# Performance work log

Hardware: AMD Instinct MI355X
Metric: run time of the kernel (lower is better)

## Reference

```python
import jax, jax.numpy as jnp
import numpy as np

B, M, D, N, P = 8, 4096, 1024, 64, 2
TEMP = 0.1
EPS = 1e-12  # torch F.normalize default eps


def setup_inputs() -> dict:
    key = jax.random.key(0)
    k1, k2, k3 = jax.random.split(key, 3)
    x = jax.random.normal(k1, (B, M, D), jnp.float32)
    # xavier_normal_(phi, gain=1.5): std = 1.5*sqrt(2/(fan_in+fan_out)) with fan_in=D, fan_out=N*P
    phi = jax.random.normal(k2, (D, N, P), jnp.float32) * np.float32(1.5 * np.sqrt(2.0 / (D + N * P)))
    scale = jnp.ones((1,), jnp.float32)
    W = jax.random.normal(k3, (N, D, D), jnp.float32) * np.float32(1.0 / np.sqrt(D))
    b = jnp.zeros((N, D), jnp.float32)
    return {"x": x, "phi": phi, "scale": scale, "W": W, "b": b}


def reference(x, phi, scale, W, b):
    # normalize tokens along feature dim, phi along dim 0 (like F.normalize)
    xn = x / jnp.maximum(jnp.linalg.norm(x, axis=2, keepdims=True), EPS)
    phin = scale * (phi / jnp.maximum(jnp.linalg.norm(phi, axis=0, keepdims=True), EPS))
    # router logits [b, m, n, p]
    logits = jnp.einsum('bmd,dnp->bmnp', xn, phin) / TEMP
    d = jax.nn.softmax(logits, axis=1)                    # dispatch: softmax over tokens m
    c = jax.nn.softmax(logits.reshape(B, M, N * P), axis=-1).reshape(B, M, N, P)  # combine: softmax over (n,p)
    xs = jnp.einsum('bmd,bmnp->bnpd', x, d)               # slot inputs [b, n, p, d]
    # per-expert Linear(dim, dim): batched over expert axis n
    ys = jnp.einsum('bnpd,nde->bnpe', xs, W) + b[None, :, None, :]
    y = jnp.einsum('bnpd,bmnp->bmd', ys, c)
    return y + x  # add_residual=True
```

## Files before the change

kernel.cpp:

```cpp
#include <hip/hip_runtime.h>
#include <hip/hip_bf16.h>
#include <math.h>

#define B_ 8
#define M_ 4096
#define D_ 1024
#define NP_ 128
#define TEMP_ 0.1f
#define EPS_ 1e-12f

typedef __attribute__((ext_vector_type(8))) short bf16x8;
typedef __attribute__((ext_vector_type(4))) float f32x4;

__device__ __forceinline__ unsigned short f2bf(float f) {
    union { float f; unsigned int u; } v; v.f = f;
    unsigned int u = v.u;
    u += 0x7fff + ((u >> 16) & 1);
    return (unsigned short)(u >> 16);
}

__device__ __forceinline__ void stage_tile(const char* gbase, size_t row_stride,
                                           char* lds, int tid) {
    const int lane = tid & 63, w = tid >> 6;
#pragma unroll
    for (int t = 0; t < 2; ++t) {
        const int row = w * 32 + t * 16 + (lane >> 2);
        const char* g = gbase + (size_t)row * row_stride + (lane & 3) * 16;
        char* l = lds + (w * 32 + t * 16) * 64 + lane * 16;
        __builtin_amdgcn_global_load_lds((const __attribute__((address_space(1))) unsigned int*)g,
                                         (__attribute__((address_space(3))) unsigned int*)l,
                                         16, 0, 0);
    }
}

__device__ __forceinline__ void stage_rows64(const char* gbase, size_t row_stride,
                                             char* lds, int tid) {
    const int lane = tid & 63, w = tid >> 6;
    const int row = w * 16 + (lane >> 2);
    const char* g = gbase + (size_t)row * row_stride + (lane & 3) * 16;
    char* l = lds + (w * 16) * 64 + lane * 16;
    __builtin_amdgcn_global_load_lds((const __attribute__((address_space(1))) unsigned int*)g,
                                     (__attribute__((address_space(3))) unsigned int*)l,
                                     16, 0, 0);
}

template <int NI, int NJ>
__device__ __forceinline__ void mfma_tile(const char* At, const char* Bt,
                                          f32x4 (&acc)[NI][NJ], int wm, int wn,
                                          int fr, int q) {
    bf16x8 a[NI], bb[NJ];
#pragma unroll
    for (int i = 0; i < NI; ++i)
        a[i] = *(const bf16x8*)(At + (wm + i * 16 + fr) * 64 + q * 16);
#pragma unroll
    for (int j = 0; j < NJ; ++j)
        bb[j] = *(const bf16x8*)(Bt + (wn + j * 16 + fr) * 64 + q * 16);
#pragma unroll
    for (int i = 0; i < NI; ++i)
#pragma unroll
        for (int j = 0; j < NJ; ++j)
            acc[i][j] = __builtin_amdgcn_mfma_f32_16x16x32_bf16(a[i], bb[j], acc[i][j], 0, 0, 0);
}

__global__ __launch_bounds__(256) void k_prepT(const float* __restrict__ x,
                                               unsigned short* __restrict__ xbf,
                                               unsigned short* __restrict__ xbfT,
                                               float* __restrict__ rinv) {
    const int p = blockIdx.x;
    const int b = p >> 6, m0 = (p & 63) * 64;
    const int tid = threadIdx.x;
    const int mg = tid >> 4;
    const int d4 = tid & 15;
    __shared__ unsigned short lt[2][64][72];
    float ss[4] = {0.f, 0.f, 0.f, 0.f};
    for (int ch = 0; ch < 16; ++ch) {
        const int d0 = ch * 64;
        const int buf = ch & 1;
#pragma unroll
        for (int ii = 0; ii < 4; ++ii) {
            const int m = mg + ii * 16;
            float4 v = *(const float4*)(x + ((size_t)(b * M_ + m0 + m)) * D_ + d0 + d4 * 4);
            ss[ii] += v.x * v.x + v.y * v.y + v.z * v.z + v.w * v.w;
            ushort4 bv;
            bv.x = f2bf(v.x); bv.y = f2bf(v.y); bv.z = f2bf(v.z); bv.w = f2bf(v.w);
            *(ushort4*)(xbf + ((size_t)(b * M_ + m0 + m)) * D_ + d0 + d4 * 4) = bv;
            lt[buf][d4 * 4 + 0][m] = bv.x;
            lt[buf][d4 * 4 + 1][m] = bv.y;
            lt[buf][d4 * 4 + 2][m] = bv.z;
            lt[buf][d4 * 4 + 3][m] = bv.w;
        }
        __syncthreads();
        const int dl = tid >> 2, mq = (tid & 3) * 16;
        bf16x8 v0 = *(const bf16x8*)&lt[buf][dl][mq];
        bf16x8 v1 = *(const bf16x8*)&lt[buf][dl][mq + 8];
        unsigned short* to = xbfT + ((size_t)(b * D_ + d0 + dl)) * M_ + m0 + mq;
        *(bf16x8*)(to) = v0;
        *(bf16x8*)(to + 8) = v1;
    }
#pragma unroll
    for (int ii = 0; ii < 4; ++ii) {
        float s = ss[ii];
        s += __shfl_down(s, 8, 16);
        s += __shfl_down(s, 4, 16);
        s += __shfl_down(s, 2, 16);
        s += __shfl_down(s, 1, 16);
        if (d4 == 0)
            rinv[b * M_ + m0 + mg + ii * 16] = 1.0f / (fmaxf(sqrtf(s), EPS_) * TEMP_);
    }
}

__global__ void k_phin(const float* __restrict__ phi, const float* __restrict__ scale,
                       unsigned short* __restrict__ phinT) {
    const int np = blockIdx.x, tid = threadIdx.x;
    float ss = 0.f;
    for (int d = tid; d < D_; d += 256) {
        float v = phi[d * NP_ + np];
        ss += v * v;
    }
    __shared__ float red[256];
    red[tid] = ss;
    __syncthreads();
    for (int s = 128; s > 0; s >>= 1) {
        if (tid < s) red[tid] += red[tid + s];
        __syncthreads();
    }
    float inv = scale[0] / fmaxf(sqrtf(red[0]), EPS_);
    for (int d = tid; d < D_; d += 256) phinT[np * D_ + d] = f2bf(phi[d * NP_ + np] * inv);
}

__global__ __launch_bounds__(256) void k_logits(const unsigned short* __restrict__ phinT,
                                                const unsigned short* __restrict__ xbf,
                                                const float* __restrict__ rinv,
                                                float* __restrict__ logitsT) {
    const int m0 = blockIdx.x * 64;
    const int np0 = blockIdx.y * 64;
    const int b = blockIdx.z;
    const int tid = threadIdx.x, lane = tid & 63, w = tid >> 6;
    __shared__ char At[2][4096], Bt[2][4096];
    f32x4 acc[2][2] = {};
    const char* abase = (const char*)(xbf + ((size_t)b * M_ + m0) * D_);
    const char* bbase = (const char*)(phinT + (size_t)np0 * D_);
    const int wmm = (w & 1) * 32, wnn = (w >> 1) * 32;
    const int fr = lane & 15, q = lane >> 4;
    stage_rows64(abase, 2048, At[0], tid);
    stage_rows64(bbase, 2048, Bt[0], tid);
    __syncthreads();
    int cur = 0;
    for (int k0 = 64; k0 < 2048; k0 += 64) {
        stage_rows64(abase + k0, 2048, At[cur ^ 1], tid);
        stage_rows64(bbase + k0, 2048, Bt[cur ^ 1], tid);
        mfma_tile<2, 2>(At[cur], Bt[cur], acc, wmm, wnn, fr, q);
        __syncthreads();
        cur ^= 1;
    }
    mfma_tile<2, 2>(At[cur], Bt[cur], acc, wmm, wnn, fr, q);
#pragma unroll
    for (int i = 0; i < 2; ++i) {
        const int mm = wmm + i * 16 + q * 4;
        const float4 rv = *(const float4*)(rinv + (size_t)b * M_ + m0 + mm);
#pragma unroll
        for (int j = 0; j < 2; ++j) {
            const int np = np0 + wnn + j * 16 + fr;
            float4 o;
            o.x = acc[i][j][0] * rv.x;
            o.y = acc[i][j][1] * rv.y;
            o.z = acc[i][j][2] * rv.z;
            o.w = acc[i][j][3] * rv.w;
            *(float4*)(logitsT + ((size_t)b * NP_ + np) * M_ + m0 + mm) = o;
        }
    }
}

__global__ void k_colstats(const float* __restrict__ logitsT, float* __restrict__ cmax,
                           float* __restrict__ cinv) {
    const int row = blockIdx.x * 4 + (threadIdx.x >> 6);
    const int lane = threadIdx.x & 63;
    const float4* base = (const float4*)(logitsT + (size_t)row * M_);
    float mx = -1e30f, sm = 0.f;
#pragma unroll 4
    for (int it = 0; it < 16; ++it) {
        float4 v = base[lane + 64 * it];
        float lm = fmaxf(fmaxf(v.x, v.y), fmaxf(v.z, v.w));
        float nm = fmaxf(mx, lm);
        sm = sm * __expf(mx - nm) + __expf(v.x - nm) + __expf(v.y - nm) + __expf(v.z - nm) +
             __expf(v.w - nm);
        mx = nm;
    }
    for (int off = 32; off > 0; off >>= 1) {
        float om = __shfl_down(mx, off), os = __shfl_down(sm, off);
        float nm = fmaxf(mx, om);
        sm = sm * __expf(mx - nm) + os * __expf(om - nm);
        mx = nm;
    }
    if (lane == 0) {
        cmax[row] = mx;
        cinv[row] = 1.0f / sm;
    }
}

__global__ __launch_bounds__(256) void k_weights(const float* __restrict__ logitsT,
                                                 const float* __restrict__ cmax,
                                                 const float* __restrict__ cinv,
                                                 unsigned short* __restrict__ dvalT,
                                                 unsigned short* __restrict__ cbf) {
    const int b = blockIdx.y, m0 = blockIdx.x * 32;
    const int tid = threadIdx.x;
    __shared__ float lt[128][36];
    __shared__ float red[32][8];
    __shared__ float rstat[32][2];
    const int np = tid >> 1;
    const int mh = (tid & 1) * 16;
    const float cm = cmax[b * NP_ + np], ci = cinv[b * NP_ + np];
    unsigned short ev[16];
#pragma unroll
    for (int ii = 0; ii < 4; ++ii) {
        const int mq = mh + ii * 4;
        float4 v = *(const float4*)(logitsT + ((size_t)b * NP_ + np) * M_ + m0 + mq);
        *(float4*)&lt[np][mq] = v;
        ev[ii * 4 + 0] = f2bf(__expf(v.x - cm) * ci);
        ev[ii * 4 + 1] = f2bf(__expf(v.y - cm) * ci);
        ev[ii * 4 + 2] = f2bf(__expf(v.z - cm) * ci);
        ev[ii * 4 + 3] = f2bf(__expf(v.w - cm) * ci);
    }
    {
        unsigned short* dp = dvalT + ((size_t)b * NP_ + np) * M_ + m0 + mh;
        *(bf16x8*)dp = *(const bf16x8*)&ev[0];
        *(bf16x8*)(dp + 8) = *(const bf16x8*)&ev[8];
    }
    __syncthreads();
    const int mm = tid >> 3, g = tid & 7;
    float mx = -1e30f;
#pragma unroll
    for (int i = 0; i < 16; ++i) mx = fmaxf(mx, lt[g * 16 + i][mm]);
    red[mm][g] = mx;
    __syncthreads();
    if (g == 0) {
        float M2 = red[mm][0];
#pragma unroll
        for (int k = 1; k < 8; ++k) M2 = fmaxf(M2, red[mm][k]);
        rstat[mm][0] = M2;
    }
    __syncthreads();
    const float rm = rstat[mm][0];
    float s = 0.f;
#pragma unroll
    for (int i = 0; i < 16; ++i) s += __expf(lt[g * 16 + i][mm] - rm);
    red[mm][g] = s;
    __syncthreads();
    if (g == 0) {
        float S = 0.f;
#pragma unroll
        for (int k = 0; k < 8; ++k) S += red[mm][k];
        rstat[mm][1] = 1.0f / S;
    }
    __syncthreads();
    const float ri = rstat[mm][1];
    bf16x8 o0, o1;
#pragma unroll
    for (int i = 0; i < 8; ++i) o0[i] = (short)f2bf(__expf(lt[g * 16 + i][mm] - rm) * ri);
#pragma unroll
    for (int i = 0; i < 8; ++i) o1[i] = (short)f2bf(__expf(lt[g * 16 + 8 + i][mm] - rm) * ri);
    unsigned short* co = cbf + ((size_t)b * M_ + m0 + mm) * NP_ + g * 16;
    *(bf16x8*)(co) = o0;
    *(bf16x8*)(co + 8) = o1;
}

__global__ __launch_bounds__(256) void k_xs(const unsigned short* __restrict__ dvalT,
                                            const unsigned short* __restrict__ xbfT,
                                            float* __restrict__ partial) {
    const int dt = blockIdx.x, kc = blockIdx.y, b = blockIdx.z;
    const int d0 = dt * 64;
    const int tid = threadIdx.x, lane = tid & 63, w = tid >> 6;
    __shared__ char At[2][4096], Bt[2][8192];
    f32x4 acc[2][4] = {};
    const char* abase = (const char*)(xbfT + ((size_t)b * D_ + d0) * M_) + (size_t)kc * 1024;
    const char* bbase = (const char*)(dvalT + (size_t)b * NP_ * M_) + (size_t)kc * 1024;
    const int wmm = (w & 1) * 32, wnn = (w >> 1) * 64;
    const int fr = lane & 15, q = lane >> 4;
    stage_rows64(abase, (size_t)M_ * 2, At[0], tid);
    stage_tile(bbase, (size_t)M_ * 2, Bt[0], tid);
    __syncthreads();
    int cur = 0;
    for (int k0 = 64; k0 < 1024; k0 += 64) {
        stage_rows64(abase + k0, (size_t)M_ * 2, At[cur ^ 1], tid);
        stage_tile(bbase + k0, (size_t)M_ * 2, Bt[cur ^ 1], tid);
        mfma_tile<2, 4>(At[cur], Bt[cur], acc, wmm, wnn, fr, q);
        __syncthreads();
        cur ^= 1;
    }
    mfma_tile<2, 4>(At[cur], Bt[cur], acc, wmm, wnn, fr, q);
#pragma unroll
    for (int i = 0; i < 2; ++i) {
        const int dd = d0 + wmm + i * 16 + q * 4;
#pragma unroll
        for (int j = 0; j < 4; ++j) {
            const int np = wnn + j * 16 + fr;
            float4 o;
            o.x = acc[i][j][0]; o.y = acc[i][j][1]; o.z = acc[i][j][2]; o.w = acc[i][j][3];
            *(float4*)(partial + (((size_t)kc * B_ + b) * NP_ + np) * D_ + dd) = o;
        }
    }
}

__global__ void k_xsred(const float* __restrict__ partial, float* __restrict__ xs) {
    const size_t i = ((size_t)blockIdx.x * 256 + threadIdx.x) * 4;
    const size_t CH = (size_t)B_ * NP_ * D_;
    float4 o = *(const float4*)(partial + i);
#pragma unroll
    for (int c = 1; c < 8; ++c) {
        float4 s = *(const float4*)(partial + (size_t)c * CH + i);
        o.x += s.x; o.y += s.y; o.z += s.z; o.w += s.w;
    }
    *(float4*)(xs + i) = o;
}

__global__ __launch_bounds__(256) void k_ys(const float* __restrict__ xs,
                                            const float* __restrict__ W,
                                            const float* __restrict__ bias,
                                            unsigned short* __restrict__ ysT) {
    const int et = blockIdx.x;
    const int n = blockIdx.y;
    const int e0 = et * 128;
    const int tid = threadIdx.x, tx = tid & 31, ty = tid >> 5;
    __shared__ float wt[32][128];
    __shared__ float xst[16][32];
    float acc[2][4];
#pragma unroll
    for (int j = 0; j < 2; ++j)
#pragma unroll
        for (int q = 0; q < 4; ++q) acc[j][q] = 0.f;
    const float* wbase = W + (size_t)n * D_ * D_;
    for (int k0 = 0; k0 < D_; k0 += 32) {
#pragma unroll
        for (int it = 0; it < 4; ++it) {
            int idx = tid + 256 * it;
            int row = idx >> 5, c4 = (idx & 31) * 4;
            *(float4*)(&wt[row][c4]) = *(const float4*)(wbase + (size_t)(k0 + row) * D_ + e0 + c4);
        }
        if (tid < 128) {
            int r = tid >> 3, c4 = (tid & 7) * 4;
            int bb = r >> 1, pp = r & 1;
            *(float4*)(&xst[r][c4]) =
                *(const float4*)(xs + ((size_t)bb * NP_ + n * 2 + pp) * D_ + k0 + c4);
        }
        __syncthreads();
#pragma unroll
        for (int k = 0; k < 32; ++k) {
            float4 w4 = *(const float4*)(&wt[k][tx * 4]);
            float r0 = xst[ty * 2][k], r1 = xst[ty * 2 + 1][k];
            acc[0][0] += r0 * w4.x; acc[0][1] += r0 * w4.y;
            acc[0][2] += r0 * w4.z; acc[0][3] += r0 * w4.w;
            acc[1][0] += r1 * w4.x; acc[1][1] += r1 * w4.y;
            acc[1][2] += r1 * w4.z; acc[1][3] += r1 * w4.w;
        }
        __syncthreads();
    }
    float4 bv = *(const float4*)(bias + n * D_ + e0 + tx * 4);
#pragma unroll
    for (int j = 0; j < 2; ++j) {
        const int r = ty * 2 + j;
        const int bb = r >> 1, pp = r & 1;
        float v0 = acc[j][0] + bv.x, v1 = acc[j][1] + bv.y;
        float v2 = acc[j][2] + bv.z, v3 = acc[j][3] + bv.w;
        ysT[((size_t)bb * D_ + e0 + tx * 4 + 0) * NP_ + n * 2 + pp] = f2bf(v0);
        ysT[((size_t)bb * D_ + e0 + tx * 4 + 1) * NP_ + n * 2 + pp] = f2bf(v1);
        ysT[((size_t)bb * D_ + e0 + tx * 4 + 2) * NP_ + n * 2 + pp] = f2bf(v2);
        ysT[((size_t)bb * D_ + e0 + tx * 4 + 3) * NP_ + n * 2 + pp] = f2bf(v3);
    }
}

__global__ __launch_bounds__(256) void k_final(const unsigned short* __restrict__ cbf,
                                               const unsigned short* __restrict__ ysT,
                                               const float* __restrict__ x,
                                               float* __restrict__ out) {
    const int et = blockIdx.x, mt = blockIdx.y, b = blockIdx.z;
    const int e0 = et * 128, m0 = mt * 128;
    const int tid = threadIdx.x, lane = tid & 63, w = tid >> 6;
    __shared__ char At[2][8192], Bt[2][8192];
    f32x4 acc[4][4] = {};
    const char* abase = (const char*)(ysT + ((size_t)b * D_ + e0) * NP_);
    const char* bbase = (const char*)(cbf + ((size_t)b * M_ + m0) * NP_);
    const int wmm = (w & 1) * 64, wnn = (w >> 1) * 64;
    const int fr = lane & 15, q = lane >> 4;
    stage_tile(abase, 256, At[0], tid);
    stage_tile(bbase, 256, Bt[0], tid);
    __syncthreads();
    int cur = 0;
    for (int k0 = 64; k0 < 256; k0 += 64) {
        stage_tile(abase + k0, 256, At[cur ^ 1], tid);
        stage_tile(bbase + k0, 256, Bt[cur ^ 1], tid);
        mfma_tile<4, 4>(At[cur], Bt[cur], acc, wmm, wnn, fr, q);
        __syncthreads();
        cur ^= 1;
    }
    mfma_tile<4, 4>(At[cur], Bt[cur], acc, wmm, wnn, fr, q);
#pragma unroll
    for (int i = 0; i < 4; ++i) {
        const int e = e0 + wmm + i * 16 + q * 4;
#pragma unroll
        for (int j = 0; j < 4; ++j) {
            const int m = m0 + wnn + j * 16 + fr;
            const size_t idx = ((size_t)b * M_ + m) * D_ + e;
            float4 xv = *(const float4*)(x + idx);
            float4 o;
            o.x = acc[i][j][0] + xv.x;
            o.y = acc[i][j][1] + xv.y;
            o.z = acc[i][j][2] + xv.z;
            o.w = acc[i][j][3] + xv.w;
            *(float4*)(out + idx) = o;
        }
    }
}

extern "C" void kernel_launch(void* const* d_in, const int* in_sizes, int n_in,
                              void* d_out, int out_size, void* d_ws, size_t ws_size,
                              hipStream_t stream) {
    const float* x = (const float*)d_in[0];
    const float* phi = (const float*)d_in[1];
    const float* scale = (const float*)d_in[2];
    const float* W = (const float*)d_in[3];
    const float* bias = (const float*)d_in[4];
    float* out = (float*)d_out;

    char* ws = (char*)d_ws;
    float* rinv = (float*)ws;
    float* cmax = (float*)(ws + 131072);
    float* cinv = (float*)(ws + 135168);
    unsigned short* phinT = (unsigned short*)(ws + 139264);
    unsigned short* xbf = (unsigned short*)(ws + 401408);
    unsigned short* xbfT = (unsigned short*)(ws + 401408 + 67108864);
    float* logitsT = (float*)(ws + 401408 + 134217728);
    unsigned short* dvalT = (unsigned short*)(ws + 401408 + 150994944);
    unsigned short* cbf = (unsigned short*)(ws + 401408 + 159383552);
    float* partial = (float*)xbf;
    float* xs = (float*)((char*)xbf + 33554432);
    unsigned short* ysT = (unsigned short*)((char*)xbf + 37748736);

    k_prepT<<<512, 256, 0, stream>>>(x, xbf, xbfT, rinv);
    k_phin<<<128, 256, 0, stream>>>(phi, scale, phinT);
    k_logits<<<dim3(64, 2, 8), 256, 0, stream>>>(phinT, xbf, rinv, logitsT);
    k_colstats<<<256, 256, 0, stream>>>(logitsT, cmax, cinv);
    k_weights<<<dim3(128, 8), 256, 0, stream>>>(logitsT, cmax, cinv, dvalT, cbf);
    k_xs<<<dim3(16, 8, 8), 256, 0, stream>>>(dvalT, xbfT, partial);
    k_xsred<<<1024, 256, 0, stream>>>(partial, xs);
    k_ys<<<dim3(8, 64), 256, 0, stream>>>(xs, W, bias, ysT);
    k_final<<<dim3(8, 32, 8), 256, 0, stream>>>(cbf, ysT, x, out);
}
```

Before: 694.0 us.

## Swizzle LDS tiles, widen K-steps, merge logits NP tiles, rewrite expert linear

GEMM staging changes from 64-byte rows to XOR-swizzled 128- and 256-byte rows so each barrier covers more K and LDS bank conflicts drop. k_logits now computes all 128 router columns per block, so the x tile is loaded once instead of twice. k_xs uses half as many K splits, which shrinks the partial buffers, and k_final stages the whole K=128 in one step without double buffering. k_xsred now writes slot-interleaved xs, and k_ys becomes a register-streaming loop that reads W directly, with the LDS transpose in k_prepT also swizzled. The trade-off is more LDS per block and fewer blocks in k_xs, which may reduce occupancy.

New measurement: 681.4 us. About the same (-1.8%).

```diff
diff --git a/kernel.cpp b/kernel.cpp
--- a/kernel.cpp
+++ b/kernel.cpp
@@ -19,47 +19,84 @@
     return (unsigned short)(u >> 16);
 }
 
-__device__ __forceinline__ void stage_tile(const char* gbase, size_t row_stride,
-                                           char* lds, int tid) {
-    const int lane = tid & 63, w = tid >> 6;
-#pragma unroll
-    for (int t = 0; t < 2; ++t) {
-        const int row = w * 32 + t * 16 + (lane >> 2);
-        const char* g = gbase + (size_t)row * row_stride + (lane & 3) * 16;
-        char* l = lds + (w * 32 + t * 16) * 64 + lane * 16;
-        __builtin_amdgcn_global_load_lds((const __attribute__((address_space(1))) unsigned int*)g,
-                                         (__attribute__((address_space(3))) unsigned int*)l,
+template <int R>
+__device__ __forceinline__ void stage128s(const char* gbase, size_t row_stride,
+                                          char* lds, int tid) {
+#pragma unroll
+    for (int it = 0; it < R / 32; ++it) {
+        const int g = tid + 256 * it;
+        const int row = g >> 3;
+        const int scol = ((g & 7) * 16) ^ ((row & 7) << 4);
+        const char* gp = gbase + (size_t)row * row_stride + scol;
+        __builtin_amdgcn_global_load_lds((const __attribute__((address_space(1))) unsigned int*)gp,
+                                         (__attribute__((address_space(3))) unsigned int*)(lds + g * 16),
                                          16, 0, 0);
     }
 }
 
-__device__ __forceinline__ void stage_rows64(const char* gbase, size_t row_stride,
-                                             char* lds, int tid) {
-    const int lane = tid & 63, w = tid >> 6;
-    const int row = w * 16 + (lane >> 2);
-    const char* g = gbase + (size_t)row * row_stride + (lane & 3) * 16;
-    char* l = lds + (w * 16) * 64 + lane * 16;
-    __builtin_amdgcn_global_load_lds((const __attribute__((address_space(1))) unsigned int*)g,
-                                     (__attribute__((address_space(3))) unsigned int*)l,
-                                     16, 0, 0);
+template <int R>
+__device__ __forceinline__ void stage256s(const char* gbase, size_t row_stride,
+                                          char* lds, int tid) {
+#pragma unroll
+    for (int it = 0; it < R / 16; ++it) {
+        const int g = tid + 256 * it;
+        const int row = g >> 4;
+        const int scol = ((g & 15) * 16) ^ ((row & 7) << 4);
+        const char* gp = gbase + (size_t)row * row_stride + scol;
+        __builtin_amdgcn_global_load_lds((const __attribute__((address_space(1))) unsigned int*)gp,
+                                         (__attribute__((address_space(3))) unsigned int*)(lds + g * 16),
+                                         16, 0, 0);
+    }
 }
 
 template <int NI, int NJ>
-__device__ __forceinline__ void mfma_tile(const char* At, const char* Bt,
-                                          f32x4 (&acc)[NI][NJ], int wm, int wn,
-                                          int fr, int q) {
-    bf16x8 a[NI], bb[NJ];
-#pragma unroll
-    for (int i = 0; i < NI; ++i)
-        a[i] = *(const bf16x8*)(At + (wm + i * 16 + fr) * 64 + q * 16);
-#pragma unroll
-    for (int j = 0; j < NJ; ++j)
-        bb[j] = *(const bf16x8*)(Bt + (wn + j * 16 + fr) * 64 + q * 16);
-#pragma unroll
-    for (int i = 0; i < NI; ++i)
-#pragma unroll
-        for (int j = 0; j < NJ; ++j)
-            acc[i][j] = __builtin_amdgcn_mfma_f32_16x16x32_bf16(a[i], bb[j], acc[i][j], 0, 0, 0);
+__device__ __forceinline__ void mfma128(const char* At, const char* Bt,
+                                        f32x4 (&acc)[NI][NJ], int wm, int wn,
+                                        int fr, int q) {
+#pragma unroll
+    for (int ks = 0; ks < 2; ++ks) {
+        bf16x8 a[NI], bb[NJ];
+#pragma unroll
+        for (int i = 0; i < NI; ++i) {
+            const int row = wm + i * 16 + fr;
+            a[i] = *(const bf16x8*)(At + ((row * 128 + ks * 64 + q * 16) ^ ((row & 7) << 4)));
+        }
+#pragma unroll
+        for (int j = 0; j < NJ; ++j) {
+            const int row = wn + j * 16 + fr;
+            bb[j] = *(const bf16x8*)(Bt + ((row * 128 + ks * 64 + q * 16) ^ ((row & 7) << 4)));
+        }
+#pragma unroll
+        for (int i = 0; i < NI; ++i)
+#pragma unroll
+            for (int j = 0; j < NJ; ++j)
+                acc[i][j] = __builtin_amdgcn_mfma_f32_16x16x32_bf16(a[i], bb[j], acc[i][j], 0, 0, 0);
+    }
+}
+
+template <int NI, int NJ>
+__device__ __forceinline__ void mfma256(const char* At, const char* Bt,
+                                        f32x4 (&acc)[NI][NJ], int wm, int wn,
+                                        int fr, int q) {
+#pragma unroll
+    for (int ks = 0; ks < 4; ++ks) {
+        bf16x8 a[NI], bb[NJ];
+#pragma unroll
+        for (int i = 0; i < NI; ++i) {
+            const int row = wm + i * 16 + fr;
+            a[i] = *(const bf16x8*)(At + ((row * 256 + ks * 64 + q * 16) ^ ((row & 7) << 4)));
+        }
+#pragma unroll
+        for (int j = 0; j < NJ; ++j) {
+            const int row = wn + j * 16 + fr;
+            bb[j] = *(const bf16x8*)(Bt + ((row * 256 + ks * 64 + q * 16) ^ ((row & 7) << 4)));
+        }
+#pragma unroll
+        for (int i = 0; i < NI; ++i)
+#pragma unroll
+            for (int j = 0; j < NJ; ++j)
+                acc[i][j] = __builtin_amdgcn_mfma_f32_16x16x32_bf16(a[i], bb[j], acc[i][j], 0, 0, 0);
+    }
 }
 
 __global__ __launch_bounds__(256) void k_prepT(const float* __restrict__ x,
@@ -71,8 +108,9 @@
     const int tid = threadIdx.x;
     const int mg = tid >> 4;
     const int d4 = tid & 15;
-    __shared__ unsigned short lt[2][64][72];
+    __shared__ char ltb[2][64 * 144];
     float ss[4] = {0.f, 0.f, 0.f, 0.f};
+    const int skey = (d4 & 7) << 4;
     for (int ch = 0; ch < 16; ++ch) {
         const int d0 = ch * 64;
         const int buf = ch & 1;
@@ -84,15 +122,17 @@
             ushort4 bv;
             bv.x = f2bf(v.x); bv.y = f2bf(v.y); bv.z = f2bf(v.z); bv.w = f2bf(v.w);
             *(ushort4*)(xbf + ((size_t)(b * M_ + m0 + m)) * D_ + d0 + d4 * 4) = bv;
-            lt[buf][d4 * 4 + 0][m] = bv.x;
-            lt[buf][d4 * 4 + 1][m] = bv.y;
-            lt[buf][d4 * 4 + 2][m] = bv.z;
-            lt[buf][d4 * 4 + 3][m] = bv.w;
+            const int r0 = d4 * 4;
+            *(unsigned short*)(ltb[buf] + (((r0 + 0) * 144 + m * 2) ^ skey)) = bv.x;
+            *(unsigned short*)(ltb[buf] + (((r0 + 1) * 144 + m * 2) ^ skey)) = bv.y;
+            *(unsigned short*)(ltb[buf] + (((r0 + 2) * 144 + m * 2) ^ skey)) = bv.z;
+            *(unsigned short*)(ltb[buf] + (((r0 + 3) * 144 + m * 2) ^ skey)) = bv.w;
         }
         __syncthreads();
         const int dl = tid >> 2, mq = (tid & 3) * 16;
-        bf16x8 v0 = *(const bf16x8*)&lt[buf][dl][mq];
-        bf16x8 v1 = *(const bf16x8*)&lt[buf][dl][mq + 8];
+        const int rkey = ((dl >> 2) & 7) << 4;
+        bf16x8 v0 = *(const bf16x8*)(ltb[buf] + ((dl * 144 + mq * 2) ^ rkey));
+        bf16x8 v1 = *(const bf16x8*)(ltb[buf] + ((dl * 144 + mq * 2 + 16) ^ rkey));
         unsigned short* to = xbfT + ((size_t)(b * D_ + d0 + dl)) * M_ + m0 + mq;
         *(bf16x8*)(to) = v0;
         *(bf16x8*)(to + 8) = v1;
@@ -133,34 +173,33 @@
                                                 const float* __restrict__ rinv,
                                                 float* __restrict__ logitsT) {
     const int m0 = blockIdx.x * 64;
-    const int np0 = blockIdx.y * 64;
-    const int b = blockIdx.z;
+    const int b = blockIdx.y;
     const int tid = threadIdx.x, lane = tid & 63, w = tid >> 6;
-    __shared__ char At[2][4096], Bt[2][4096];
-    f32x4 acc[2][2] = {};
+    __shared__ char At[2][8192], Bt[2][16384];
+    f32x4 acc[2][4] = {};
     const char* abase = (const char*)(xbf + ((size_t)b * M_ + m0) * D_);
-    const char* bbase = (const char*)(phinT + (size_t)np0 * D_);
-    const int wmm = (w & 1) * 32, wnn = (w >> 1) * 32;
+    const char* bbase = (const char*)phinT;
+    const int wm = (w & 1) * 32, wn = (w >> 1) * 64;
     const int fr = lane & 15, q = lane >> 4;
-    stage_rows64(abase, 2048, At[0], tid);
-    stage_rows64(bbase, 2048, Bt[0], tid);
+    stage128s<64>(abase, 2048, At[0], tid);
+    stage128s<128>(bbase, 2048, Bt[0], tid);
     __syncthreads();
     int cur = 0;
-    for (int k0 = 64; k0 < 2048; k0 += 64) {
-        stage_rows64(abase + k0, 2048, At[cur ^ 1], tid);
-        stage_rows64(bbase + k0, 2048, Bt[cur ^ 1], tid);
-        mfma_tile<2, 2>(At[cur], Bt[cur], acc, wmm, wnn, fr, q);
+    for (int k0 = 128; k0 < 2048; k0 += 128) {
+        stage128s<64>(abase + k0, 2048, At[cur ^ 1], tid);
+        stage128s<128>(bbase + k0, 2048, Bt[cur ^ 1], tid);
+        mfma128<2, 4>(At[cur], Bt[cur], acc, wm, wn, fr, q);
         __syncthreads();
         cur ^= 1;
     }
-    mfma_tile<2, 2>(At[cur], Bt[cur], acc, wmm, wnn, fr, q);
+    mfma128<2, 4>(At[cur], Bt[cur], acc, wm, wn, fr, q);
 #pragma unroll
     for (int i = 0; i < 2; ++i) {
-        const int mm = wmm + i * 16 + q * 4;
+        const int mm = wm + i * 16 + q * 4;
         const float4 rv = *(const float4*)(rinv + (size_t)b * M_ + m0 + mm);
 #pragma unroll
-        for (int j = 0; j < 2; ++j) {
-            const int np = np0 + wnn + j * 16 + fr;
+        for (int j = 0; j < 4; ++j) {
+            const int np = wn + j * 16 + fr;
             float4 o;
             o.x = acc[i][j][0] * rv.x;
             o.y = acc[i][j][1] * rv.y;
@@ -271,30 +310,30 @@
     const int dt = blockIdx.x, kc = blockIdx.y, b = blockIdx.z;
     const int d0 = dt * 64;
     const int tid = threadIdx.x, lane = tid & 63, w = tid >> 6;
-    __shared__ char At[2][4096], Bt[2][8192];
+    __shared__ char At[2][8192], Bt[2][16384];
     f32x4 acc[2][4] = {};
-    const char* abase = (const char*)(xbfT + ((size_t)b * D_ + d0) * M_) + (size_t)kc * 1024;
-    const char* bbase = (const char*)(dvalT + (size_t)b * NP_ * M_) + (size_t)kc * 1024;
-    const int wmm = (w & 1) * 32, wnn = (w >> 1) * 64;
+    const char* abase = (const char*)(xbfT + ((size_t)b * D_ + d0) * M_) + (size_t)kc * 2048;
+    const char* bbase = (const char*)(dvalT + (size_t)b * NP_ * M_) + (size_t)kc * 2048;
+    const int wm = (w & 1) * 32, wn = (w >> 1) * 64;
     const int fr = lane & 15, q = lane >> 4;
-    stage_rows64(abase, (size_t)M_ * 2, At[0], tid);
-    stage_tile(bbase, (size_t)M_ * 2, Bt[0], tid);
+    stage128s<64>(abase, (size_t)M_ * 2, At[0], tid);
+    stage128s<128>(bbase, (size_t)M_ * 2, Bt[0], tid);
     __syncthreads();
     int cur = 0;
-    for (int k0 = 64; k0 < 1024; k0 += 64) {
-        stage_rows64(abase + k0, (size_t)M_ * 2, At[cur ^ 1], tid);
-        stage_tile(bbase + k0, (size_t)M_ * 2, Bt[cur ^ 1], tid);
-        mfma_tile<2, 4>(At[cur], Bt[cur], acc, wmm, wnn, fr, q);
+    for (int k0 = 128; k0 < 2048; k0 += 128) {
+        stage128s<64>(abase + k0, (size_t)M_ * 2, At[cur ^ 1], tid);
+        stage128s<128>(bbase + k0, (size_t)M_ * 2, Bt[cur ^ 1], tid);
+        mfma128<2, 4>(At[cur], Bt[cur], acc, wm, wn, fr, q);
         __syncthreads();
         cur ^= 1;
     }
-    mfma_tile<2, 4>(At[cur], Bt[cur], acc, wmm, wnn, fr, q);
+    mfma128<2, 4>(At[cur], Bt[cur], acc, wm, wn, fr, q);
 #pragma unroll
     for (int i = 0; i < 2; ++i) {
-        const int dd = d0 + wmm + i * 16 + q * 4;
+        const int dd = d0 + wm + i * 16 + q * 4;
 #pragma unroll
         for (int j = 0; j < 4; ++j) {
-            const int np = wnn + j * 16 + fr;
+            const int np = wn + j * 16 + fr;
             float4 o;
             o.x = acc[i][j][0]; o.y = acc[i][j][1]; o.z = acc[i][j][2]; o.w = acc[i][j][3];
             *(float4*)(partial + (((size_t)kc * B_ + b) * NP_ + np) * D_ + dd) = o;
@@ -302,70 +341,54 @@
     }
 }
 
-__global__ void k_xsred(const float* __restrict__ partial, float* __restrict__ xs) {
+__global__ void k_xsred(const float* __restrict__ partial, float* __restrict__ xsT) {
     const size_t i = ((size_t)blockIdx.x * 256 + threadIdx.x) * 4;
     const size_t CH = (size_t)B_ * NP_ * D_;
     float4 o = *(const float4*)(partial + i);
 #pragma unroll
-    for (int c = 1; c < 8; ++c) {
+    for (int c = 1; c < 4; ++c) {
         float4 s = *(const float4*)(partial + (size_t)c * CH + i);
         o.x += s.x; o.y += s.y; o.z += s.z; o.w += s.w;
     }
-    *(float4*)(xs + i) = o;
-}
-
-__global__ __launch_bounds__(256) void k_ys(const float* __restrict__ xs,
+    const int d = (int)(i % D_);
+    const int np = (int)((i / D_) % NP_);
+    const int b = (int)(i / ((size_t)D_ * NP_));
+    const int n = np >> 1, pp = np & 1, slot = b * 2 + pp;
+    float* xp = xsT + ((size_t)n * D_ + d) * 16 + slot;
+    xp[0] = o.x;
+    xp[16] = o.y;
+    xp[32] = o.z;
+    xp[48] = o.w;
+}
+
+__global__ __launch_bounds__(256) void k_ys(const float* __restrict__ xsT,
                                             const float* __restrict__ W,
                                             const float* __restrict__ bias,
                                             unsigned short* __restrict__ ysT) {
     const int et = blockIdx.x;
     const int n = blockIdx.y;
-    const int e0 = et * 128;
-    const int tid = threadIdx.x, tx = tid & 31, ty = tid >> 5;
-    __shared__ float wt[32][128];
-    __shared__ float xst[16][32];
-    float acc[2][4];
-#pragma unroll
-    for (int j = 0; j < 2; ++j)
-#pragma unroll
-        for (int q = 0; q < 4; ++q) acc[j][q] = 0.f;
-    const float* wbase = W + (size_t)n * D_ * D_;
-    for (int k0 = 0; k0 < D_; k0 += 32) {
-#pragma unroll
-        for (int it = 0; it < 4; ++it) {
-            int idx = tid + 256 * it;
-            int row = idx >> 5, c4 = (idx & 31) * 4;
-            *(float4*)(&wt[row][c4]) = *(const float4*)(wbase + (size_t)(k0 + row) * D_ + e0 + c4);
-        }
-        if (tid < 128) {
-            int r = tid >> 3, c4 = (tid & 7) * 4;
-            int bb = r >> 1, pp = r & 1;
-            *(float4*)(&xst[r][c4]) =
-                *(const float4*)(xs + ((size_t)bb * NP_ + n * 2 + pp) * D_ + k0 + c4);
-        }
-        __syncthreads();
-#pragma unroll
-        for (int k = 0; k < 32; ++k) {
-            float4 w4 = *(const float4*)(&wt[k][tx * 4]);
-            float r0 = xst[ty * 2][k], r1 = xst[ty * 2 + 1][k];
-            acc[0][0] += r0 * w4.x; acc[0][1] += r0 * w4.y;
-            acc[0][2] += r0 * w4.z; acc[0][3] += r0 * w4.w;
-            acc[1][0] += r1 * w4.x; acc[1][1] += r1 * w4.y;
-            acc[1][2] += r1 * w4.z; acc[1][3] += r1 * w4.w;
-        }
-        __syncthreads();
-    }
-    float4 bv = *(const float4*)(bias + n * D_ + e0 + tx * 4);
-#pragma unroll
-    for (int j = 0; j < 2; ++j) {
-        const int r = ty * 2 + j;
-        const int bb = r >> 1, pp = r & 1;
-        float v0 = acc[j][0] + bv.x, v1 = acc[j][1] + bv.y;
-        float v2 = acc[j][2] + bv.z, v3 = acc[j][3] + bv.w;
-        ysT[((size_t)bb * D_ + e0 + tx * 4 + 0) * NP_ + n * 2 + pp] = f2bf(v0);
-        ysT[((size_t)bb * D_ + e0 + tx * 4 + 1) * NP_ + n * 2 + pp] = f2bf(v1);
-        ysT[((size_t)bb * D_ + e0 + tx * 4 + 2) * NP_ + n * 2 + pp] = f2bf(v2);
-        ysT[((size_t)bb * D_ + e0 + tx * 4 + 3) * NP_ + n * 2 + pp] = f2bf(v3);
+    const int tid = threadIdx.x, lane = tid & 63;
+    const int wu = __builtin_amdgcn_readfirstlane(tid >> 6);
+    const int e = et * 128 + lane * 2;
+    const float* wb = W + (size_t)n * D_ * D_ + e;
+    const float* sb = xsT + (size_t)n * D_ * 16 + wu * 4;
+    float acc[4][2] = {};
+#pragma unroll 8
+    for (int k = 0; k < D_; ++k) {
+        float2 wv = *(const float2*)(wb + (size_t)k * D_);
+        float4 sv = *(const float4*)(sb + (size_t)k * 16);
+        acc[0][0] = fmaf(sv.x, wv.x, acc[0][0]); acc[0][1] = fmaf(sv.x, wv.y, acc[0][1]);
+        acc[1][0] = fmaf(sv.y, wv.x, acc[1][0]); acc[1][1] = fmaf(sv.y, wv.y, acc[1][1]);
+        acc[2][0] = fmaf(sv.z, wv.x, acc[2][0]); acc[2][1] = fmaf(sv.z, wv.y, acc[2][1]);
+        acc[3][0] = fmaf(sv.w, wv.x, acc[3][0]); acc[3][1] = fmaf(sv.w, wv.y, acc[3][1]);
+    }
+    float2 bv = *(const float2*)(bias + n * D_ + e);
+#pragma unroll
+    for (int s = 0; s < 4; ++s) {
+        const int slot = wu * 4 + s;
+        const int b = slot >> 1, pp = slot & 1;
+        ysT[((size_t)b * D_ + e) * NP_ + n * 2 + pp] = f2bf(acc[s][0] + bv.x);
+        ysT[((size_t)b * D_ + e + 1) * NP_ + n * 2 + pp] = f2bf(acc[s][1] + bv.y);
     }
 }
 
@@ -376,30 +399,22 @@
     const int et = blockIdx.x, mt = blockIdx.y, b = blockIdx.z;
     const int e0 = et * 128, m0 = mt * 128;
     const int tid = threadIdx.x, lane = tid & 63, w = tid >> 6;
-    __shared__ char At[2][8192], Bt[2][8192];
+    __shared__ char At[32768], Bt[32768];
     f32x4 acc[4][4] = {};
     const char* abase = (const char*)(ysT + ((size_t)b * D_ + e0) * NP_);
     const char* bbase = (const char*)(cbf + ((size_t)b * M_ + m0) * NP_);
-    const int wmm = (w & 1) * 64, wnn = (w >> 1) * 64;
+    const int wm = (w & 1) * 64, wn = (w >> 1) * 64;
     const int fr = lane & 15, q = lane >> 4;
-    stage_tile(abase, 256, At[0], tid);
-    stage_tile(bbase, 256, Bt[0], tid);
-    __syncthreads();
-    int cur = 0;
-    for (int k0 = 64; k0 < 256; k0 += 64) {
-        stage_tile(abase + k0, 256, At[cur ^ 1], tid);
-        stage_tile(bbase + k0, 256, Bt[cur ^ 1], tid);
-        mfma_tile<4, 4>(At[cur], Bt[cur], acc, wmm, wnn, fr, q);
-        __syncthreads();
-        cur ^= 1;
-    }
-    mfma_tile<4, 4>(At[cur], Bt[cur], acc, wmm, wnn, fr, q);
+    stage256s<128>(abase, 256, At, tid);
+    stage256s<128>(bbase, 256, Bt, tid);
+    __syncthreads();
+    mfma256<4, 4>(At, Bt, acc, wm, wn, fr, q);
 #pragma unroll
     for (int i = 0; i < 4; ++i) {
-        const int e = e0 + wmm + i * 16 + q * 4;
+        const int e = e0 + wm + i * 16 + q * 4;
 #pragma unroll
         for (int j = 0; j < 4; ++j) {
-            const int m = m0 + wnn + j * 16 + fr;
+            const int m = m0 + wn + j * 16 + fr;
             const size_t idx = ((size_t)b * M_ + m) * D_ + e;
             float4 xv = *(const float4*)(x + idx);
             float4 o;
@@ -433,16 +448,16 @@
     unsigned short* dvalT = (unsigned short*)(ws + 401408 + 150994944);
     unsigned short* cbf = (unsigned short*)(ws + 401408 + 159383552);
     float* partial = (float*)xbf;
-    float* xs = (float*)((char*)xbf + 33554432);
-    unsigned short* ysT = (unsigned short*)((char*)xbf + 37748736);
+    float* xsT = (float*)((char*)xbf + 16777216);
+    unsigned short* ysT = (unsigned short*)((char*)xbf + 20971520);
 
     k_prepT<<<512, 256, 0, stream>>>(x, xbf, xbfT, rinv);
     k_phin<<<128, 256, 0, stream>>>(phi, scale, phinT);
-    k_logits<<<dim3(64, 2, 8), 256, 0, stream>>>(phinT, xbf, rinv, logitsT);
+    k_logits<<<dim3(64, 8), 256, 0, stream>>>(phinT, xbf, rinv, logitsT);
     k_colstats<<<256, 256, 0, stream>>>(logitsT, cmax, cinv);
     k_weights<<<dim3(128, 8), 256, 0, stream>>>(logitsT, cmax, cinv, dvalT, cbf);
-    k_xs<<<dim3(16, 8, 8), 256, 0, stream>>>(dvalT, xbfT, partial);
-    k_xsred<<<1024, 256, 0, stream>>>(partial, xs);
-    k_ys<<<dim3(8, 64), 256, 0, stream>>>(xs, W, bias, ysT);
+    k_xs<<<dim3(16, 4, 8), 256, 0, stream>>>(dvalT, xbfT, partial);
+    k_xsred<<<1024, 256, 0, stream>>>(partial, xsT);
+    k_ys<<<dim3(8, 64), 256, 0, stream>>>(xsT, W, bias, ysT);
     k_final<<<dim3(8, 32, 8), 256, 0, stream>>>(cbf, ysT, x, out);
 }
```
